# Optimization experiments

Hardware: AMD Instinct MI355X
Metric: run time of the kernel (lower is better)

Reference implementation:

```python
import jax, jax.numpy as jnp
import numpy as np

TEMP_DIV = 13.0  # forward hard-codes attn / 13 (self.temperature is unused)


def setup_inputs() -> dict:
    key = jax.random.key(0)
    k1, k2, k3 = jax.random.split(key, 3)
    B, Lq, Lk, D = 8, 2048, 2048, 640
    q = jax.random.normal(k1, (B, Lq, D), dtype=jnp.float32)
    k = jax.random.normal(k2, (B, Lk, D), dtype=jnp.float32)
    v = jax.random.normal(k3, (B, Lk, D), dtype=jnp.float32)
    return {"q": q, "k": k, "v": v}


def _l2_scores(q, k):
    # -sum((q[:,:,None,:] - k[:,None,:,:])**2, axis=3) via the GEMM expansion
    # ||q||^2 - 2 q.k + ||k||^2  -> avoids the (B,Lq,Lk,D) intermediate.
    qq = jnp.sum(q * q, axis=-1)            # (B, Lq)
    kk = jnp.sum(k * k, axis=-1)            # (B, Lk)
    qk = jnp.einsum('bqd,bkd->bqk', q, k)   # (B, Lq, Lk)
    return -(qq[:, :, None] - 2.0 * qk + kk[:, None, :])


def reference(q, k, v):
    attn_logits = _l2_scores(q, k) / TEMP_DIV          # (B, Lq, Lk)
    log_attn = jax.nn.log_softmax(attn_logits, axis=2)
    attn = jnp.exp(log_attn)                            # softmax, shares the stable pass
    # dropout is identity in eval mode
    output = jnp.einsum('bqk,bkd->bqd', attn, v)        # bmm
    return (output, attn, log_attn)
```

## Files before the change

kernel.cpp:

```cpp
#include <hip/hip_runtime.h>


#define B_   8
#define LQ   2048
#define LK   2048
#define DD   640

typedef short s16x8 __attribute__((ext_vector_type(8)));
typedef float f32x4 __attribute__((ext_vector_type(4)));

__device__ __forceinline__ unsigned short f2bf(float x) {
    unsigned int u = __float_as_uint(x);
    unsigned int r = (u + 0x7fffu + ((u >> 16) & 1u)) >> 16;
    return (unsigned short)r;
}

__global__ __launch_bounds__(256) void cvt_norm2(const float* __restrict__ q,
                                                 const float* __restrict__ k,
                                                 unsigned short* __restrict__ q16,
                                                 unsigned short* __restrict__ k16,
                                                 float* __restrict__ qq,
                                                 float* __restrict__ kkn) {
    int row  = blockIdx.x * 4 + (threadIdx.x >> 6);
    int lane = threadIdx.x & 63;
    const float* src;
    unsigned short* dst;
    float* nrm;
    int r;
    if (row < B_ * LQ) { src = q; dst = q16; nrm = qq;  r = row; }
    else               { src = k; dst = k16; nrm = kkn; r = row - B_ * LQ; }
    const float4* s = (const float4*)(src + (size_t)r * DD);
    unsigned short* d = dst + (size_t)r * DD;
    float ss = 0.f;
    for (int t = lane; t < DD / 4; t += 64) {
        float4 x = s[t];
        ss += x.x * x.x + x.y * x.y + x.z * x.z + x.w * x.w;
        ushort4 o;
        o.x = f2bf(x.x); o.y = f2bf(x.y); o.z = f2bf(x.z); o.w = f2bf(x.w);
        *(ushort4*)(d + t * 4) = o;
    }
    #pragma unroll
    for (int o = 32; o; o >>= 1) ss += __shfl_xor(ss, o);
    if (lane == 0) nrm[r] = ss;
}

__global__ __launch_bounds__(256) void cvt_transpose_v(const float* __restrict__ v,
                                                       unsigned short* __restrict__ vt) {
    __shared__ float tile[64][65];
    int bx = blockIdx.x;
    int b  = bx / 320;
    int r  = bx % 320;
    int tj = r / 10;
    int td = r % 10;
    const float* src = v + (size_t)b * LK * DD + (size_t)tj * 64 * DD + td * 64;
    for (int e = threadIdx.x; e < 4096; e += 256) {
        int rr = e >> 6, cc = e & 63;
        tile[rr][cc] = src[(size_t)rr * DD + cc];
    }
    __syncthreads();
    unsigned short* dst = vt + (size_t)b * DD * LK + (size_t)td * 64 * LK + tj * 64;
    for (int e = threadIdx.x; e < 4096; e += 256) {
        int rr = e >> 6, cc = e & 63;
        dst[(size_t)rr * LK + cc] = f2bf(tile[cc][rr]);
    }
}

template <int LDAB, int KSZ, int NTN, bool EPI>
__global__ __launch_bounds__(256) void gemm_nt(
    const unsigned short* __restrict__ A, const unsigned short* __restrict__ Bm,
    float* __restrict__ C, size_t strideA, size_t strideB, size_t strideC, int ldc,
    const float* __restrict__ qq, const float* __restrict__ kkn) {
    __shared__ unsigned short lA[128 * 64];
    __shared__ unsigned short lB[128 * 64];
    __shared__ float snm[256];

    constexpr int G = NTN * 2;
    int bx = blockIdx.x;
    int x  = bx & 7;
    int i  = bx >> 3;
    int b  = i / G;
    int j  = i % G;
    int tn = j >> 1;
    int tm = (x << 1) | (j & 1);

    const unsigned short* Ab = A + b * strideA + (size_t)tm * 128 * LDAB;
    const unsigned short* Bb = Bm + b * strideB + (size_t)tn * 128 * LDAB;

    int tid = threadIdx.x;
    int wave = tid >> 6, lane = tid & 63;

    if (EPI) {
        if (tid < 128) snm[tid] = qq[b * LQ + tm * 128 + tid];
        else           snm[tid] = kkn[b * LK + tn * 128 + (tid - 128)];
    }

    f32x4 acc[4][4] = {};
    int wm = wave >> 1, wn = wave & 1;
    int lrow = lane & 15;
    int lk8  = (lane >> 4) * 8;
    int srow = lane >> 3;
    int scol = (lane & 7) * 8;

    for (int k0 = 0; k0 < KSZ; k0 += 64) {
        __syncthreads();
        #pragma unroll
        for (int c = 0; c < 4; ++c) {
            int rbase = (c * 4 + wave) * 8;
            __builtin_amdgcn_global_load_lds(
                (const __attribute__((address_space(1))) void*)(Ab + (size_t)(rbase + srow) * LDAB + k0 + scol),
                (__attribute__((address_space(3))) void*)(lA + rbase * 64), 16, 0, 0);
            __builtin_amdgcn_global_load_lds(
                (const __attribute__((address_space(1))) void*)(Bb + (size_t)(rbase + srow) * LDAB + k0 + scol),
                (__attribute__((address_space(3))) void*)(lB + rbase * 64), 16, 0, 0);
        }
        __syncthreads();
        #pragma unroll
        for (int kk = 0; kk < 64; kk += 32) {
            s16x8 af[4], bf[4];
            #pragma unroll
            for (int t = 0; t < 4; ++t)
                af[t] = *(const s16x8*)(lA + (wm * 64 + t * 16 + lrow) * 64 + kk + lk8);
            #pragma unroll
            for (int t = 0; t < 4; ++t)
                bf[t] = *(const s16x8*)(lB + (wn * 64 + t * 16 + lrow) * 64 + kk + lk8);
            #pragma unroll
            for (int mt = 0; mt < 4; ++mt)
                #pragma unroll
                for (int nt = 0; nt < 4; ++nt)
                    acc[mt][nt] = __builtin_amdgcn_mfma_f32_16x16x32_bf16(
                        af[mt], bf[nt], acc[mt][nt], 0, 0, 0);
        }
    }

    float* Cb = C + b * strideC + (size_t)(tm * 128) * ldc + tn * 128;
    #pragma unroll
    for (int mt = 0; mt < 4; ++mt)
        #pragma unroll
        for (int nt = 0; nt < 4; ++nt) {
            int col = wn * 64 + nt * 16 + lrow;
            int rb  = wm * 64 + mt * 16 + ((lane >> 4) << 2);
            #pragma unroll
            for (int rr = 0; rr < 4; ++rr) {
                float val = acc[mt][nt][rr];
                if (EPI) val = (2.0f * val - snm[rb + rr] - snm[128 + col]) * (1.0f / 13.0f);
                Cb[(size_t)(rb + rr) * ldc + col] = val;
            }
        }
}

__global__ __launch_bounds__(256) void softmax_fix(float* __restrict__ logits,
                                                   float* __restrict__ attn,
                                                   unsigned short* __restrict__ a16) {
    __shared__ float redm[4], reds[4];
    size_t row = blockIdx.x;
    float* Lr = logits + row * LK;
    int tid = threadIdx.x;
    float x[8];
    *(float4*)(x)     = *(const float4*)(Lr + tid * 8);
    *(float4*)(x + 4) = *(const float4*)(Lr + tid * 8 + 4);

    float m = x[0];
    #pragma unroll
    for (int i = 1; i < 8; ++i) m = fmaxf(m, x[i]);
    #pragma unroll
    for (int o = 32; o; o >>= 1) m = fmaxf(m, __shfl_xor(m, o));
    int wv = tid >> 6, ln = tid & 63;
    if (ln == 0) redm[wv] = m;
    __syncthreads();
    m = fmaxf(fmaxf(redm[0], redm[1]), fmaxf(redm[2], redm[3]));

    float e[8];
    float s = 0.f;
    #pragma unroll
    for (int i = 0; i < 8; ++i) { e[i] = __expf(x[i] - m); s += e[i]; }
    #pragma unroll
    for (int o = 32; o; o >>= 1) s += __shfl_xor(s, o);
    if (ln == 0) reds[wv] = s;
    __syncthreads();
    s = reds[0] + reds[1] + reds[2] + reds[3];

    float lse = __logf(s);
    float inv = 1.0f / s;
    float at[8], la[8];
    #pragma unroll
    for (int i = 0; i < 8; ++i) { at[i] = e[i] * inv; la[i] = x[i] - m - lse; }

    float* Ar = attn + row * LK;
    *(float4*)(Ar + tid * 8)     = *(float4*)at;
    *(float4*)(Ar + tid * 8 + 4) = *(float4*)(at + 4);
    *(float4*)(Lr + tid * 8)     = *(float4*)la;
    *(float4*)(Lr + tid * 8 + 4) = *(float4*)(la + 4);

    unsigned short h[8];
    #pragma unroll
    for (int i = 0; i < 8; ++i) h[i] = f2bf(at[i]);
    unsigned short* Hr = a16 + row * LK;
    *(ushort4*)(Hr + tid * 8)     = *(ushort4*)h;
    *(ushort4*)(Hr + tid * 8 + 4) = *(ushort4*)(h + 4);
}

extern "C" void kernel_launch(void* const* d_in, const int* in_sizes, int n_in,
                              void* d_out, int out_size, void* d_ws, size_t ws_size,
                              hipStream_t stream) {
    const float* q = (const float*)d_in[0];
    const float* k = (const float*)d_in[1];
    const float* v = (const float*)d_in[2];

    float* out   = (float*)d_out;
    float* attn  = out + (size_t)B_ * LQ * DD;
    float* logat = attn + (size_t)B_ * LQ * LK;

    unsigned short* q16  = (unsigned short*)d_ws;
    unsigned short* k16  = q16 + (size_t)B_ * LQ * DD;
    unsigned short* v16t = k16 + (size_t)B_ * LK * DD;
    unsigned short* a16  = v16t + (size_t)B_ * DD * LK;
    float* qq  = (float*)(a16 + (size_t)B_ * LQ * LK);
    float* kkn = qq + (size_t)B_ * LQ;

    cvt_norm2<<<2 * B_ * LQ / 4, 256, 0, stream>>>(q, k, q16, k16, qq, kkn);
    cvt_transpose_v<<<B_ * (LK / 64) * (DD / 64), 256, 0, stream>>>(v, v16t);

    gemm_nt<DD, DD, 16, true><<<B_ * 16 * 16, 256, 0, stream>>>(
        q16, k16, logat,
        (size_t)LQ * DD, (size_t)LK * DD, (size_t)LQ * LK, LK, qq, kkn);

    softmax_fix<<<B_ * LQ, 256, 0, stream>>>(logat, attn, a16);

    gemm_nt<LK, LK, 5, false><<<B_ * 16 * 5, 256, 0, stream>>>(
        a16, v16t, out,
        (size_t)LQ * LK, (size_t)DD * LK, (size_t)LQ * DD, DD, nullptr, nullptr);
}
```

Measured before the change: 626.3 us.

## Rewrite GEMMs as 256-row double-buffered pipelined kernels with swizzled LDS

Both GEMMs now use a new kernel with 512 threads and 256-row tiles (256 or 128 columns). It double-buffers LDS and issues global-to-LDS loads two k-steps ahead, gated by explicit vmcnt waits, and XOR-swizzles the LDS layout to avoid bank conflicts. It also raises MFMA priority with setprio and reads the norms directly from global memory in the epilogue. The aim is to hide load latency and raise reuse per tile, at the cost of fewer blocks (lower occupancy and wave count) and fragile hand-counted waitcnts.

```diff
diff --git a/kernel.cpp b/kernel.cpp
--- a/kernel.cpp
+++ b/kernel.cpp
@@ -65,87 +65,139 @@
     }
 }
 
-template <int LDAB, int KSZ, int NTN, bool EPI>
-__global__ __launch_bounds__(256) void gemm_nt(
+template <int LDA, int LDB, int KSZ, int NTN, int BN, int WM, int WN, bool EPI>
+__global__ __launch_bounds__(512, 2) void gemm_nt256(
     const unsigned short* __restrict__ A, const unsigned short* __restrict__ Bm,
     float* __restrict__ C, size_t strideA, size_t strideB, size_t strideC, int ldc,
     const float* __restrict__ qq, const float* __restrict__ kkn) {
-    __shared__ unsigned short lA[128 * 64];
-    __shared__ unsigned short lB[128 * 64];
-    __shared__ float snm[256];
-
-    constexpr int G = NTN * 2;
+
+    constexpr int KT   = KSZ / 64;
+    constexpr int RM   = 256 / WM / 16;
+    constexpr int RN   = BN  / WN / 16;
+    constexpr int LBLD = BN / 64;
+
+    __shared__ unsigned short lA[2 * 2 * 256 * 32];
+    __shared__ unsigned short lB[2 * 2 * BN  * 32];
+
     int bx = blockIdx.x;
-    int x  = bx & 7;
+    int tm = bx & 7;
     int i  = bx >> 3;
-    int b  = i / G;
-    int j  = i % G;
-    int tn = j >> 1;
-    int tm = (x << 1) | (j & 1);
-
-    const unsigned short* Ab = A + b * strideA + (size_t)tm * 128 * LDAB;
-    const unsigned short* Bb = Bm + b * strideB + (size_t)tn * 128 * LDAB;
-
-    int tid = threadIdx.x;
-    int wave = tid >> 6, lane = tid & 63;
-
-    if (EPI) {
-        if (tid < 128) snm[tid] = qq[b * LQ + tm * 128 + tid];
-        else           snm[tid] = kkn[b * LK + tn * 128 + (tid - 128)];
-    }
-
-    f32x4 acc[4][4] = {};
-    int wm = wave >> 1, wn = wave & 1;
+    int tn = i % NTN;
+    int b  = i / NTN;
+
+    const unsigned short* Ab = A  + b * strideA + (size_t)tm * 256 * LDA;
+    const unsigned short* Bb = Bm + b * strideB + (size_t)tn * BN  * LDB;
+
+    int tid  = threadIdx.x;
+    int w    = tid >> 6;
+    int lane = tid & 63;
     int lrow = lane & 15;
-    int lk8  = (lane >> 4) * 8;
-    int srow = lane >> 3;
-    int scol = (lane & 7) * 8;
-
-    for (int k0 = 0; k0 < KSZ; k0 += 64) {
-        __syncthreads();
-        #pragma unroll
-        for (int c = 0; c < 4; ++c) {
-            int rbase = (c * 4 + wave) * 8;
+    int lk4  = lane >> 4;
+    int wm   = w / WN;
+    int wn   = w % WN;
+
+    auto stage = [&](int kt, int p) {
+        int k0 = kt * 64;
+        #pragma unroll
+        for (int s = 0; s < 4; ++s) {
+            int row = ((s & 1) << 7) | (tid >> 2);
+            int kh  = s >> 1;
+            int ch  = tid & 3;
+            int sc  = k0 + kh * 32 + ((ch ^ ((row >> 1) & 3)) << 3);
             __builtin_amdgcn_global_load_lds(
-                (const __attribute__((address_space(1))) void*)(Ab + (size_t)(rbase + srow) * LDAB + k0 + scol),
-                (__attribute__((address_space(3))) void*)(lA + rbase * 64), 16, 0, 0);
+                (const __attribute__((address_space(1))) void*)(Ab + (size_t)row * LDA + sc),
+                (__attribute__((address_space(3))) void*)(lA + p * 16384 + s * 4096 + w * 512),
+                16, 0, 0);
+        }
+        #pragma unroll
+        for (int s = 0; s < LBLD; ++s) {
+            int o  = s * 8192 + tid * 16;
+            int kh = o / (BN * 64);
+            int rr = (o & (BN * 64 - 1)) >> 6;
+            int ch = (o >> 4) & 3;
+            int sc = k0 + kh * 32 + ((ch ^ ((rr >> 1) & 3)) << 3);
             __builtin_amdgcn_global_load_lds(
-                (const __attribute__((address_space(1))) void*)(Bb + (size_t)(rbase + srow) * LDAB + k0 + scol),
-                (__attribute__((address_space(3))) void*)(lB + rbase * 64), 16, 0, 0);
-        }
-        __syncthreads();
-        #pragma unroll
-        for (int kk = 0; kk < 64; kk += 32) {
-            s16x8 af[4], bf[4];
-            #pragma unroll
-            for (int t = 0; t < 4; ++t)
-                af[t] = *(const s16x8*)(lA + (wm * 64 + t * 16 + lrow) * 64 + kk + lk8);
-            #pragma unroll
-            for (int t = 0; t < 4; ++t)
-                bf[t] = *(const s16x8*)(lB + (wn * 64 + t * 16 + lrow) * 64 + kk + lk8);
-            #pragma unroll
-            for (int mt = 0; mt < 4; ++mt)
+                (const __attribute__((address_space(1))) void*)(Bb + (size_t)rr * LDB + sc),
+                (__attribute__((address_space(3))) void*)(lB + p * (BN * 64) + s * 4096 + w * 512),
+                16, 0, 0);
+        }
+    };
+
+    f32x4 acc[RM][RN] = {};
+
+    stage(0, 0);
+    stage(1, 1);
+
+    #pragma unroll 2
+    for (int t = 0; t < KT; ++t) {
+        int p = t & 1;
+        if constexpr (BN == 256) asm volatile("s_waitcnt vmcnt(8)" ::: "memory");
+        else                     asm volatile("s_waitcnt vmcnt(6)" ::: "memory");
+        __builtin_amdgcn_s_barrier();
+        __builtin_amdgcn_sched_barrier(0);
+        asm volatile("" ::: "memory");
+
+        const unsigned short* pA = lA + p * 16384;
+        const unsigned short* pB = lB + p * (BN * 64);
+
+        s16x8 bf[RN][2];
+        #pragma unroll
+        for (int n = 0; n < RN; ++n)
+            #pragma unroll
+            for (int kh = 0; kh < 2; ++kh) {
+                int br = wn * (RN * 16) + n * 16 + lrow;
+                bf[n][kh] = *(const s16x8*)(pB + kh * (BN * 32) + br * 32 +
+                                            ((lk4 ^ ((br >> 1) & 3)) << 3));
+            }
+
+        #pragma unroll
+        for (int qm = 0; qm < 2; ++qm) {
+            s16x8 af[RM / 2][2];
+            #pragma unroll
+            for (int m = 0; m < RM / 2; ++m)
                 #pragma unroll
-                for (int nt = 0; nt < 4; ++nt)
-                    acc[mt][nt] = __builtin_amdgcn_mfma_f32_16x16x32_bf16(
-                        af[mt], bf[nt], acc[mt][nt], 0, 0, 0);
-        }
-    }
-
-    float* Cb = C + b * strideC + (size_t)(tm * 128) * ldc + tn * 128;
-    #pragma unroll
-    for (int mt = 0; mt < 4; ++mt)
-        #pragma unroll
-        for (int nt = 0; nt < 4; ++nt) {
-            int col = wn * 64 + nt * 16 + lrow;
-            int rb  = wm * 64 + mt * 16 + ((lane >> 4) << 2);
+                for (int kh = 0; kh < 2; ++kh) {
+                    int ar = wm * (RM * 16) + (qm * (RM / 2) + m) * 16 + lrow;
+                    af[m][kh] = *(const s16x8*)(pA + kh * 8192 + ar * 32 +
+                                                ((lk4 ^ ((ar >> 1) & 3)) << 3));
+                }
+            __builtin_amdgcn_s_setprio(1);
+            #pragma unroll
+            for (int kh = 0; kh < 2; ++kh)
+                #pragma unroll
+                for (int m = 0; m < RM / 2; ++m)
+                    #pragma unroll
+                    for (int n = 0; n < RN; ++n)
+                        acc[qm * (RM / 2) + m][n] = __builtin_amdgcn_mfma_f32_16x16x32_bf16(
+                            af[m][kh], bf[n][kh], acc[qm * (RM / 2) + m][n], 0, 0, 0);
+            __builtin_amdgcn_s_setprio(0);
+        }
+
+        asm volatile("" ::: "memory");
+        __builtin_amdgcn_sched_barrier(0);
+        __builtin_amdgcn_s_barrier();
+        int t2 = (t + 2 < KT) ? t + 2 : 0;
+        stage(t2, p);
+    }
+    asm volatile("s_waitcnt vmcnt(0)" ::: "memory");
+
+    float* Cb = C + b * strideC + (size_t)(tm * 256) * ldc + tn * BN;
+    #pragma unroll
+    for (int mi = 0; mi < RM; ++mi) {
+        int rb = wm * (RM * 16) + mi * 16 + lk4 * 4;
+        #pragma unroll
+        for (int ni = 0; ni < RN; ++ni) {
+            int col = wn * (RN * 16) + ni * 16 + lrow;
             #pragma unroll
             for (int rr = 0; rr < 4; ++rr) {
-                float val = acc[mt][nt][rr];
-                if (EPI) val = (2.0f * val - snm[rb + rr] - snm[128 + col]) * (1.0f / 13.0f);
+                float val = acc[mi][ni][rr];
+                if constexpr (EPI)
+                    val = (2.0f * val - qq[b * LQ + tm * 256 + rb + rr]
+                                      - kkn[b * LK + tn * BN + col]) * (1.0f / 13.0f);
                 Cb[(size_t)(rb + rr) * ldc + col] = val;
             }
         }
+    }
 }
 
 __global__ __launch_bounds__(256) void softmax_fix(float* __restrict__ logits,
@@ -220,13 +272,13 @@
     cvt_norm2<<<2 * B_ * LQ / 4, 256, 0, stream>>>(q, k, q16, k16, qq, kkn);
     cvt_transpose_v<<<B_ * (LK / 64) * (DD / 64), 256, 0, stream>>>(v, v16t);
 
-    gemm_nt<DD, DD, 16, true><<<B_ * 16 * 16, 256, 0, stream>>>(
+    gemm_nt256<DD, DD, DD, 8, 256, 2, 4, true><<<B_ * 8 * 8, 512, 0, stream>>>(
         q16, k16, logat,
         (size_t)LQ * DD, (size_t)LK * DD, (size_t)LQ * LK, LK, qq, kkn);
 
     softmax_fix<<<B_ * LQ, 256, 0, stream>>>(logat, attn, a16);
 
-    gemm_nt<LK, LK, 5, false><<<B_ * 16 * 5, 256, 0, stream>>>(
+    gemm_nt256<LK, LK, LK, 5, 128, 4, 2, false><<<B_ * 8 * 5, 512, 0, stream>>>(
         a16, v16t, out,
         (size_t)LQ * LK, (size_t)DD * LK, (size_t)LQ * DD, DD, nullptr, nullptr);
 }
```

New measurement: 616.2 us. Within noise of the previous version (-1.6%).
